# Performance work log

Hardware: AMD Instinct MI355X
Metric: run time of the kernel (lower is better)

The kernel has to match this reference:

```python
import jax, jax.numpy as jnp
import numpy as np

S, N, D_IN, D_GNN, E = 8, 50000, 128, 128, 1600000


def setup_inputs() -> dict:
    key = jax.random.key(0)
    k = jax.random.split(key, 7)
    inp = jax.random.normal(k[0], (S, N, D_IN), dtype=jnp.float32)
    edge_index = jax.random.randint(k[1], (2, E), 0, N, dtype=jnp.int64)
    # SAGEConv params: lin_l (neighbor branch, with bias), lin_r (root, no bias)
    s_in = 1.0 / np.sqrt(D_IN)
    W_l = jax.random.uniform(k[2], (D_GNN, D_IN), jnp.float32, -s_in, s_in)
    b_l = jax.random.uniform(k[3], (D_GNN,), jnp.float32, -s_in, s_in)
    W_r = jax.random.uniform(k[4], (D_GNN, D_IN), jnp.float32, -s_in, s_in)
    s_g = 1.0 / np.sqrt(D_GNN)
    W_fc = jax.random.uniform(k[5], (1, D_GNN), jnp.float32, -s_g, s_g)
    b_fc = jax.random.uniform(k[6], (1,), jnp.float32, -s_g, s_g)
    return {"input": inp, "edge_index": edge_index, "W_l": W_l, "b_l": b_l,
            "W_r": W_r, "W_fc": W_fc, "b_fc": b_fc}


def reference(input, edge_index, W_l, b_l, W_r, W_fc, b_fc):
    src, dst = edge_index[0], edge_index[1]
    n = input.shape[1]
    # in-degree for mean aggregation (isolated nodes -> divide by 1, agg stays 0)
    deg = jax.ops.segment_sum(jnp.ones(src.shape[0], input.dtype), dst,
                              num_segments=n)
    deg = jnp.maximum(deg, 1.0)[:, None]

    def step(xt):  # xt: [N, D_IN]
        agg = jax.ops.segment_sum(xt[src], dst, num_segments=n) / deg
        # SAGEConv: lin_l(mean_agg) + lin_r(x)
        return agg @ W_l.T + b_l + xt @ W_r.T  # [N, D_GNN]

    xs = jax.vmap(step)(input)                   # [S, N, D_GNN]
    ys = (xs @ W_fc.T + b_fc)[..., 0]            # [S, N]
    return xs, ys
```

## Files before the change

kernel.cpp:

```cpp
#include <hip/hip_runtime.h>

#define S_STEPS 8
#define D 128

typedef __attribute__((ext_vector_type(4))) float f32x4;
typedef __attribute__((ext_vector_type(4))) short s16x4;
typedef __attribute__((ext_vector_type(8))) short s16x8;

static __device__ __forceinline__ short f2bf(float f) {
    union { float f; unsigned u; } x; x.f = f;
    unsigned r = x.u + 0x7fffu + ((x.u >> 16) & 1u);
    return (short)(r >> 16);
}

__global__ void count_kernel(const int* __restrict__ dst, int* __restrict__ cnt, int E) {
    int e = blockIdx.x * blockDim.x + threadIdx.x;
    if (e < E) atomicAdd(&cnt[dst[e]], 1);
}

__global__ void cvtw_kernel(const float* __restrict__ Wl, const float* __restrict__ Wr,
                            unsigned short* __restrict__ wbf) {
    int i = blockIdx.x * blockDim.x + threadIdx.x;
    if (i < 256 * 128) {
        int j = i >> 7, k = i & 127;
        float v = (j < 128) ? Wl[j * 128 + k] : Wr[(j - 128) * 128 + k];
        wbf[i] = (unsigned short)f2bf(v);
    }
}

__global__ __launch_bounds__(1024) void scan_kernel(const int* __restrict__ cnt,
                            int* __restrict__ row_ptr,
                            int* __restrict__ fill, float* __restrict__ rdeg,
                            int N, int E) {
    __shared__ int wsum[16];
    __shared__ int woff[16];
    __shared__ int carry_s;
    const int tid = threadIdx.x;
    const int lane = tid & 63;
    const int wv = tid >> 6;
    if (tid == 0) carry_s = 0;
    __syncthreads();
    for (int base = 0; base < N; base += 1024) {
        int i = base + tid;
        int v = (i < N) ? cnt[i] : 0;
        int inc = v;
#pragma unroll
        for (int off = 1; off < 64; off <<= 1) {
            int t = __shfl_up(inc, off);
            if (lane >= off) inc += t;
        }
        if (lane == 63) wsum[wv] = inc;
        __syncthreads();
        if (wv == 0 && lane < 16) {
            int s = wsum[lane];
            int in2 = s;
#pragma unroll
            for (int off = 1; off < 16; off <<= 1) {
                int t = __shfl_up(in2, off);
                if (lane >= off) in2 += t;
            }
            woff[lane] = in2 - s;
        }
        __syncthreads();
        int carry = carry_s;
        int excl = carry + woff[wv] + inc - v;
        if (i < N) {
            row_ptr[i] = excl;
            fill[i] = excl;
            rdeg[i] = 1.0f / (float)((v > 1) ? v : 1);
        }
        __syncthreads();
        if (tid == 1023) carry_s = carry + woff[15] + inc;
        __syncthreads();
    }
    if (tid == 0) row_ptr[N] = E;
}

__global__ void fill_kernel(const int* __restrict__ src, const int* __restrict__ dst,
                            int* __restrict__ fill, int* __restrict__ eidx, int E) {
    int e = blockIdx.x * blockDim.x + threadIdx.x;
    if (e < E) {
        int p = atomicAdd(&fill[dst[e]], 1);
        eidx[p] = src[e];
    }
}

__global__ __launch_bounds__(256) void lin_kernel(const float* __restrict__ x,
    const unsigned short* __restrict__ wbf, const float* __restrict__ bl,
    unsigned short* __restrict__ hbf, float* __restrict__ outb, int N)
{
    __shared__ __align__(16) short As[64 * 136];
    __shared__ float bls[128];

    const int tid = threadIdx.x;
    const int row0 = blockIdx.x * 64;
    const int lane = tid & 63;
    const int w = tid >> 6;
    const int m = lane & 15;
    const int q = lane >> 4;

    s16x8 bf[4][4];
#pragma unroll
    for (int ct = 0; ct < 4; ++ct) {
#pragma unroll
        for (int kc = 0; kc < 4; ++kc) {
            int col = (w * 4 + ct) * 16 + m;
            bf[ct][kc] = *(const s16x8*)(wbf + (size_t)col * 128 + kc * 32 + q * 8);
        }
    }
    if (tid < 128) bls[tid] = bl[tid];

#pragma unroll
    for (int it = 0; it < 8; ++it) {
        int i = tid + it * 256;
        int r = i >> 5;
        int kq = i & 31;
        int grow = row0 + r;
        float4 v = make_float4(0.f, 0.f, 0.f, 0.f);
        if (grow < N) v = *(const float4*)(x + (size_t)grow * 128 + kq * 4);
        s16x4 a; a.x = f2bf(v.x); a.y = f2bf(v.y); a.z = f2bf(v.z); a.w = f2bf(v.w);
        *(s16x4*)&As[r * 136 + kq * 4] = a;
    }
    __syncthreads();

    f32x4 acc[4][4];
#pragma unroll
    for (int i = 0; i < 4; ++i)
#pragma unroll
        for (int j = 0; j < 4; ++j) acc[i][j] = (f32x4){0.f, 0.f, 0.f, 0.f};

#pragma unroll
    for (int mt = 0; mt < 4; ++mt) {
        s16x8 af[4];
#pragma unroll
        for (int kc = 0; kc < 4; ++kc)
            af[kc] = *(const s16x8*)&As[(mt * 16 + m) * 136 + kc * 32 + q * 8];
#pragma unroll
        for (int ct = 0; ct < 4; ++ct)
#pragma unroll
            for (int kc = 0; kc < 4; ++kc)
                acc[mt][ct] = __builtin_amdgcn_mfma_f32_16x16x32_bf16(
                    af[kc], bf[ct][kc], acc[mt][ct], 0, 0, 0);
    }

    const int colbase = w * 64;
#pragma unroll
    for (int mt = 0; mt < 4; ++mt) {
        const int rowbase = row0 + mt * 16 + q * 4;
#pragma unroll
        for (int ct = 0; ct < 4; ++ct) {
            int col = colbase + ct * 16 + m;
#pragma unroll
            for (int r = 0; r < 4; ++r) {
                int rr = rowbase + r;
                if (rr < N) {
                    if (col < 128) {
                        hbf[(size_t)rr * 128 + col] = (unsigned short)f2bf(acc[mt][ct][r]);
                    } else {
                        outb[(size_t)rr * 128 + (col - 128)] = acc[mt][ct][r] + bls[col - 128];
                    }
                }
            }
        }
    }
}

__global__ __launch_bounds__(256) void agg_kernel(const unsigned short* __restrict__ hbf,
    const int* __restrict__ row_ptr, const int* __restrict__ eidx,
    const float* __restrict__ rdeg, const float* __restrict__ wfc,
    const float* __restrict__ bfc, float* __restrict__ outb,
    float* __restrict__ ys, int N)
{
    const int lane = threadIdx.x & 63;
    const int wv = threadIdx.x >> 6;
    const int node = blockIdx.x * 4 + wv;
    if (node >= N) return;
    const int g = lane >> 4;
    const int l = lane & 15;
    const int beg = row_ptr[node];
    const int end = row_ptr[node + 1];

    float acc[8];
#pragma unroll
    for (int j = 0; j < 8; ++j) acc[j] = 0.f;

    const unsigned short* hb = hbf + l * 8;
#pragma unroll 2
    for (int e = beg + g; e < end; e += 4) {
        int s = eidx[e];
        uint4 pk = *(const uint4*)(hb + (size_t)s * 128);
        union { unsigned u; float f; } t;
        t.u = pk.x << 16;        acc[0] += t.f;
        t.u = pk.x & 0xffff0000u; acc[1] += t.f;
        t.u = pk.y << 16;        acc[2] += t.f;
        t.u = pk.y & 0xffff0000u; acc[3] += t.f;
        t.u = pk.z << 16;        acc[4] += t.f;
        t.u = pk.z & 0xffff0000u; acc[5] += t.f;
        t.u = pk.w << 16;        acc[6] += t.f;
        t.u = pk.w & 0xffff0000u; acc[7] += t.f;
    }
#pragma unroll
    for (int j = 0; j < 8; ++j) {
        acc[j] += __shfl_xor(acc[j], 16);
        acc[j] += __shfl_xor(acc[j], 32);
    }
    float ax = (g == 0) ? acc[0] : (g == 1) ? acc[2] : (g == 2) ? acc[4] : acc[6];
    float ay = (g == 0) ? acc[1] : (g == 1) ? acc[3] : (g == 2) ? acc[5] : acc[7];

    const int feat = l * 8 + g * 2;
    const float rd = rdeg[node];
    const float2 base = *(const float2*)(outb + (size_t)node * 128 + feat);
    float ox = base.x + ax * rd;
    float oy = base.y + ay * rd;
    *(float2*)(outb + (size_t)node * 128 + feat) = make_float2(ox, oy);

    const float2 wv2 = *(const float2*)(wfc + feat);
    float p = ox * wv2.x + oy * wv2.y;
#pragma unroll
    for (int off = 32; off > 0; off >>= 1) p += __shfl_down(p, off);
    if (lane == 0) ys[node] = p + bfc[0];
}

extern "C" void kernel_launch(void* const* d_in, const int* in_sizes, int n_in,
                              void* d_out, int out_size, void* d_ws, size_t ws_size,
                              hipStream_t stream)
{
    const float* x   = (const float*)d_in[0];
    const int*   ei  = (const int*)d_in[1];
    const float* Wl  = (const float*)d_in[2];
    const float* bl  = (const float*)d_in[3];
    const float* Wr  = (const float*)d_in[4];
    const float* Wfc = (const float*)d_in[5];
    const float* bfc = (const float*)d_in[6];

    const int N = in_sizes[0] / (S_STEPS * D);
    const int E = in_sizes[1] / 2;
    const int* srcp = ei;
    const int* dstp = ei + E;

    char* p = (char*)d_ws;
    auto alloc = [&](size_t bytes) {
        char* r = p;
        p += (bytes + 255) & ~(size_t)255;
        return r;
    };
    int*   cnt     = (int*)alloc((size_t)N * 4);
    int*   row_ptr = (int*)alloc((size_t)(N + 1) * 4);
    int*   fill    = (int*)alloc((size_t)N * 4);
    float* rdeg    = (float*)alloc((size_t)N * 4);
    int*   eidx    = (int*)alloc((size_t)E * 4);
    unsigned short* hbf = (unsigned short*)alloc((size_t)N * D * 2);
    unsigned short* wbf = (unsigned short*)alloc((size_t)256 * 128 * 2);
    (void)ws_size;

    float* xs    = (float*)d_out;
    float* ysall = xs + (size_t)S_STEPS * N * D;

    hipMemsetAsync(cnt, 0, (size_t)N * 4, stream);
    cvtw_kernel<<<128, 256, 0, stream>>>(Wl, Wr, wbf);
    count_kernel<<<(E + 255) / 256, 256, 0, stream>>>(dstp, cnt, E);
    scan_kernel<<<1, 1024, 0, stream>>>(cnt, row_ptr, fill, rdeg, N, E);
    fill_kernel<<<(E + 255) / 256, 256, 0, stream>>>(srcp, dstp, fill, eidx, E);

    const int gl = (N + 63) / 64;
    const int ga = (N + 3) / 4;
    for (int t = 0; t < S_STEPS; ++t) {
        const float* xt = x + (size_t)t * N * D;
        float* outb = xs + (size_t)t * N * D;
        lin_kernel<<<gl, 256, 0, stream>>>(xt, wbf, bl, hbf, outb, N);
        agg_kernel<<<ga, 256, 0, stream>>>(hbf, row_ptr, eidx, rdeg, Wfc, bfc,
                                           outb, ysall + (size_t)t * N, N);
    }
}
```

Baseline: 1.170 ms.

## Interleave per-step bf16 projections and aggregate all steps in one gather pass

The linear kernel now writes its bf16 neighbor projection into a node-major buffer that interleaves all 8 time steps. A new agg8 kernel walks each node's CSR edge list once and gathers a contiguous 2 KB row per neighbor covering every step, instead of repeating the irregular gather and index reads 8 times. Each lane then accumulates 16 features for one step, adds them to the root branch, and computes the fc output. This needs a workspace 8x larger for the projections and falls back to the old per-step path when the workspace is too small.

```diff
diff --git a/kernel.cpp b/kernel.cpp
--- a/kernel.cpp
+++ b/kernel.cpp
@@ -87,7 +87,8 @@
 
 __global__ __launch_bounds__(256) void lin_kernel(const float* __restrict__ x,
     const unsigned short* __restrict__ wbf, const float* __restrict__ bl,
-    unsigned short* __restrict__ hbf, float* __restrict__ outb, int N)
+    unsigned short* __restrict__ hbf, float* __restrict__ outb, int N,
+    int SF, int tf)
 {
     __shared__ __align__(16) short As[64 * 136];
     __shared__ float bls[128];
@@ -155,7 +156,8 @@
                 int rr = rowbase + r;
                 if (rr < N) {
                     if (col < 128) {
-                        hbf[(size_t)rr * 128 + col] = (unsigned short)f2bf(acc[mt][ct][r]);
+                        hbf[((size_t)rr * SF + tf) * 128 + col] =
+                            (unsigned short)f2bf(acc[mt][ct][r]);
                     } else {
                         outb[(size_t)rr * 128 + (col - 128)] = acc[mt][ct][r] + bls[col - 128];
                     }
@@ -163,6 +165,87 @@
             }
         }
     }
+}
+
+#define BF2ACC(u, j) { union { unsigned v; float f; } lo_, hi_; \
+    lo_.v = (u) << 16; hi_.v = (u) & 0xffff0000u; \
+    acc[j] += lo_.f; acc[(j) + 1] += hi_.f; }
+#define ACC8(p, j) { BF2ACC((p).x, (j)); BF2ACC((p).y, (j) + 2); \
+    BF2ACC((p).z, (j) + 4); BF2ACC((p).w, (j) + 6); }
+
+__global__ __launch_bounds__(256) void agg8_kernel(const unsigned short* __restrict__ hbf,
+    const int* __restrict__ row_ptr, const int* __restrict__ eidx,
+    const float* __restrict__ rdeg, const float* __restrict__ wfc,
+    const float* __restrict__ bfc, float* __restrict__ xs,
+    float* __restrict__ ys, int N)
+{
+    const int lane = threadIdx.x & 63;
+    const int wv = threadIdx.x >> 6;
+    const int node = blockIdx.x * 4 + wv;
+    if (node >= N) return;
+
+    const int beg = row_ptr[node];
+    const int end = row_ptr[node + 1];
+
+    float acc[16];
+#pragma unroll
+    for (int j = 0; j < 16; ++j) acc[j] = 0.f;
+
+    const uint4* hb = (const uint4*)hbf;
+
+    int e = beg;
+    for (; e + 2 <= end; e += 2) {
+        int s0 = eidx[e];
+        int s1 = eidx[e + 1];
+        const uint4* q0 = hb + (size_t)s0 * 128 + lane * 2;
+        const uint4* q1 = hb + (size_t)s1 * 128 + lane * 2;
+        uint4 a0 = q0[0];
+        uint4 a1 = q0[1];
+        uint4 b0 = q1[0];
+        uint4 b1 = q1[1];
+        ACC8(a0, 0); ACC8(a1, 8);
+        ACC8(b0, 0); ACC8(b1, 8);
+    }
+    if (e < end) {
+        int s0 = eidx[e];
+        const uint4* q0 = hb + (size_t)s0 * 128 + lane * 2;
+        uint4 a0 = q0[0];
+        uint4 a1 = q0[1];
+        ACC8(a0, 0); ACC8(a1, 8);
+    }
+
+    const int t = lane >> 3;
+    const int fb = (lane & 7) * 16;
+    const float rd = rdeg[node];
+
+    float* orow = xs + ((size_t)t * N + node) * 128 + fb;
+    float4 o[4];
+#pragma unroll
+    for (int j = 0; j < 4; ++j) o[j] = *((const float4*)orow + j);
+#pragma unroll
+    for (int j = 0; j < 4; ++j) {
+        o[j].x += acc[j * 4 + 0] * rd;
+        o[j].y += acc[j * 4 + 1] * rd;
+        o[j].z += acc[j * 4 + 2] * rd;
+        o[j].w += acc[j * 4 + 3] * rd;
+    }
+#pragma unroll
+    for (int j = 0; j < 4; ++j) {
+        f32x4 ov = {o[j].x, o[j].y, o[j].z, o[j].w};
+        __builtin_nontemporal_store(ov, (f32x4*)orow + j);
+    }
+
+    const float4* wv4 = (const float4*)(wfc + fb);
+    float p = 0.f;
+#pragma unroll
+    for (int j = 0; j < 4; ++j) {
+        float4 w4 = wv4[j];
+        p += o[j].x * w4.x + o[j].y * w4.y + o[j].z * w4.z + o[j].w * w4.w;
+    }
+    p += __shfl_xor(p, 1);
+    p += __shfl_xor(p, 2);
+    p += __shfl_xor(p, 4);
+    if ((lane & 7) == 0) ys[(size_t)t * N + node] = p + bfc[0];
 }
 
 __global__ __launch_bounds__(256) void agg_kernel(const unsigned short* __restrict__ hbf,
@@ -249,14 +332,17 @@
     int*   fill    = (int*)alloc((size_t)N * 4);
     float* rdeg    = (float*)alloc((size_t)N * 4);
     int*   eidx    = (int*)alloc((size_t)E * 4);
-    unsigned short* hbf = (unsigned short*)alloc((size_t)N * D * 2);
     unsigned short* wbf = (unsigned short*)alloc((size_t)256 * 128 * 2);
-    (void)ws_size;
+
+    size_t used = (size_t)(p - (char*)d_ws);
+    size_t need8 = (size_t)N * S_STEPS * D * 2;
+    bool fused = (ws_size >= used + need8 + 4096);
+    unsigned short* hbf = (unsigned short*)alloc(fused ? need8 : (size_t)N * D * 2);
 
     float* xs    = (float*)d_out;
     float* ysall = xs + (size_t)S_STEPS * N * D;
 
-    hipMemsetAsync(cnt, 0, (size_t)N * 4, stream);
+    (void)hipMemsetAsync(cnt, 0, (size_t)N * 4, stream);
     cvtw_kernel<<<128, 256, 0, stream>>>(Wl, Wr, wbf);
     count_kernel<<<(E + 255) / 256, 256, 0, stream>>>(dstp, cnt, E);
     scan_kernel<<<1, 1024, 0, stream>>>(cnt, row_ptr, fill, rdeg, N, E);
@@ -264,11 +350,22 @@
 
     const int gl = (N + 63) / 64;
     const int ga = (N + 3) / 4;
-    for (int t = 0; t < S_STEPS; ++t) {
-        const float* xt = x + (size_t)t * N * D;
-        float* outb = xs + (size_t)t * N * D;
-        lin_kernel<<<gl, 256, 0, stream>>>(xt, wbf, bl, hbf, outb, N);
-        agg_kernel<<<ga, 256, 0, stream>>>(hbf, row_ptr, eidx, rdeg, Wfc, bfc,
-                                           outb, ysall + (size_t)t * N, N);
-    }
-}
+    if (fused) {
+        for (int t = 0; t < S_STEPS; ++t) {
+            const float* xt = x + (size_t)t * N * D;
+            float* outb = xs + (size_t)t * N * D;
+            lin_kernel<<<gl, 256, 0, stream>>>(xt, wbf, bl, hbf, outb, N,
+                                               S_STEPS, t);
+        }
+        agg8_kernel<<<ga, 256, 0, stream>>>(hbf, row_ptr, eidx, rdeg, Wfc, bfc,
+                                            xs, ysall, N);
+    } else {
+        for (int t = 0; t < S_STEPS; ++t) {
+            const float* xt = x + (size_t)t * N * D;
+            float* outb = xs + (size_t)t * N * D;
+            lin_kernel<<<gl, 256, 0, stream>>>(xt, wbf, bl, hbf, outb, N, 1, 0);
+            agg_kernel<<<ga, 256, 0, stream>>>(hbf, row_ptr, eidx, rdeg, Wfc, bfc,
+                                               outb, ysall + (size_t)t * N, N);
+        }
+    }
+}
```

Measured after the change: 1.244 ms. 6.4% more time.
